# Optimization experiments

Measured on AMD Instinct MI355X. Metric: run time of the kernel, lower is better.

The kernel has to match this reference:

```python
import math
import jax, jax.numpy as jnp
import numpy as np

V, D, H, L, F, T, B = 32000, 1024, 16, 4, 4096, 1024, 2
HD = D // H
EPS = 1e-5


def make_pe(max_len, d):
    pos = np.arange(max_len)[:, None].astype(np.float32)
    div = np.exp(np.arange(0, d, 2).astype(np.float32) * (-math.log(10000.0) / d))
    pe = np.zeros((max_len, d), dtype=np.float32)
    pe[:, 0::2] = np.sin(pos * div)
    pe[:, 1::2] = np.cos(pos * div)
    return jnp.asarray(pe)


def setup_inputs() -> dict:
    key = jax.random.key(0)
    ks = jax.random.split(key, 12)
    s = 0.02
    inp = {
        'tokens': jax.random.randint(ks[0], (B, T), 0, V, dtype=jnp.int32),
        'mask': jnp.tril(jnp.ones((T, T), dtype=jnp.int32)),
        'emb': jax.random.normal(ks[1], (V, D), jnp.float32) * s,
        'pe': make_pe(T, D),
        'ln1_g': jnp.ones((L, D)), 'ln1_b': jnp.zeros((L, D)),
        'Wqkv': jax.random.normal(ks[2], (L, D, 3 * D), jnp.float32) * s,
        'bqkv': jnp.zeros((L, 3 * D)),
        'Wproj': jax.random.normal(ks[3], (L, D, D), jnp.float32) * s,
        'bproj': jnp.zeros((L, D)),
        'ln2_g': jnp.ones((L, D)), 'ln2_b': jnp.zeros((L, D)),
        'W1': jax.random.normal(ks[4], (L, D, F), jnp.float32) * s,
        'b1': jnp.zeros((L, F)),
        'W2': jax.random.normal(ks[5], (L, F, D), jnp.float32) * s,
        'b2': jnp.zeros((L, D)),
        'lnf_g': jnp.ones((D,)), 'lnf_b': jnp.zeros((D,)),
        'out_b': jnp.zeros((V,)),
    }
    return inp


def layer_norm(x, g, b):
    m = jnp.mean(x, axis=-1, keepdims=True)
    v = jnp.mean((x - m) ** 2, axis=-1, keepdims=True)
    return (x - m) / jnp.sqrt(v + EPS) * g + b


def attention(x, mask, Wqkv, bqkv, Wproj, bproj):
    b, t, c = x.shape
    qkv = (x @ Wqkv + bqkv).reshape(b, t, 3, H, HD)
    q, k, v = jnp.moveaxis(qkv, 2, 0)  # each [B,T,H,HD]
    q = q.transpose(0, 2, 1, 3)  # [B,H,T,HD]
    k = k.transpose(0, 2, 1, 3)
    v = v.transpose(0, 2, 1, 3)
    scores = jnp.einsum('bhqd,bhkd->bhqk', q, k) / math.sqrt(HD)
    scores = jnp.where(mask[None, None] == 0, -1e9, scores)
    attn = jax.nn.softmax(scores, axis=-1)
    out = jnp.einsum('bhqk,bhkd->bhqd', attn, v)
    out = out.transpose(0, 2, 1, 3).reshape(b, t, c)
    return out @ Wproj + bproj, attn


def reference(tokens, mask, emb, pe, ln1_g, ln1_b, Wqkv, bqkv, Wproj, bproj,
              ln2_g, ln2_b, W1, b1, W2, b2, lnf_g, lnf_b, out_b):
    x = emb[tokens] + pe[:tokens.shape[1]]
    attn = None
    for i in range(L):
        a, attn = attention(layer_norm(x, ln1_g[i], ln1_b[i]), mask,
                            Wqkv[i], bqkv[i], Wproj[i], bproj[i])
        x = x + a
        h = layer_norm(x, ln2_g[i], ln2_b[i])
        h = jax.nn.gelu(h @ W1[i] + b1[i], approximate=False) @ W2[i] + b2[i]
        x = x + h
    x = layer_norm(x, lnf_g, lnf_b)
    logits = x @ emb.T + out_b  # weight tying
    return logits, attn
```

## Files before the change

### kernel.cpp

```cpp
#include <hip/hip_runtime.h>
#include <cstdint>

#define DEV static __device__ __forceinline__

typedef unsigned short u16;
typedef __bf16 bf16x8 __attribute__((ext_vector_type(8)));
typedef float f32x4 __attribute__((ext_vector_type(4)));
typedef unsigned short u16x4 __attribute__((ext_vector_type(4)));

constexpr int V = 32000, D = 1024, H = 16, L = 4, F = 4096, T = 1024, B = 2;
constexpr int HD = 64;

DEV u16 f2bf(float f) {
    union { float f; uint32_t i; } c; c.f = f;
    uint32_t x = c.i;
    return (u16)((x + 0x7fffu + ((x >> 16) & 1u)) >> 16);
}
DEV bf16x8 ld8(const u16* p) { return *reinterpret_cast<const bf16x8*>(p); }

DEV void gl16(const void* g, void* l) {
    __builtin_amdgcn_global_load_lds((const __attribute__((address_space(1))) void*)g,
                                     (__attribute__((address_space(3))) void*)l, 16, 0, 0);
}

__global__ __launch_bounds__(256) void k_embln(const int* __restrict__ tok,
        const float* __restrict__ emb, const float* __restrict__ pe,
        const float* __restrict__ g, const float* __restrict__ b,
        float* __restrict__ x, u16* __restrict__ out) {
    int row = blockIdx.x, tid = threadIdx.x;
    int t = row & (T - 1);
    int vv = tok[row];
    f32x4 v = ((const f32x4*)(emb + (size_t)vv * D))[tid] + ((const f32x4*)(pe + (size_t)t * D))[tid];
    ((f32x4*)(x + (size_t)row * D))[tid] = v;
    float s = v[0] + v[1] + v[2] + v[3];
    float s2 = v[0]*v[0] + v[1]*v[1] + v[2]*v[2] + v[3]*v[3];
#pragma unroll
    for (int m = 1; m < 64; m <<= 1) { s += __shfl_xor(s, m); s2 += __shfl_xor(s2, m); }
    __shared__ float ps[4], ps2[4];
    int wave = tid >> 6;
    if ((tid & 63) == 0) { ps[wave] = s; ps2[wave] = s2; }
    __syncthreads();
    s = ps[0] + ps[1] + ps[2] + ps[3];
    s2 = ps2[0] + ps2[1] + ps2[2] + ps2[3];
    float mean = s * (1.f / D);
    float var = s2 * (1.f / D) - mean * mean;
    float r = rsqrtf(var + 1e-5f);
    f32x4 gg = ((const f32x4*)g)[tid];
    f32x4 bb = ((const f32x4*)b)[tid];
    u16x4 o;
#pragma unroll
    for (int j = 0; j < 4; j++) o[j] = f2bf((v[j] - mean) * r * gg[j] + bb[j]);
    ((u16x4*)(out + (size_t)row * D))[tid] = o;
}

template <int S>
__global__ __launch_bounds__(256) void k_redln(const float* __restrict__ pp,
        const float* __restrict__ bias, float* __restrict__ x,
        const float* __restrict__ g, const float* __restrict__ b,
        u16* __restrict__ out) {
    int row = blockIdx.x, tid = threadIdx.x;
    f32x4 v = ((const f32x4*)(x + (size_t)row * D))[tid];
#pragma unroll
    for (int s = 0; s < S; s++)
        v += ((const f32x4*)(pp + ((size_t)s * (B * T) + row) * D))[tid];
    v += ((const f32x4*)bias)[tid];
    ((f32x4*)(x + (size_t)row * D))[tid] = v;
    float s = v[0] + v[1] + v[2] + v[3];
    float s2 = v[0]*v[0] + v[1]*v[1] + v[2]*v[2] + v[3]*v[3];
#pragma unroll
    for (int m = 1; m < 64; m <<= 1) { s += __shfl_xor(s, m); s2 += __shfl_xor(s2, m); }
    __shared__ float ps[4], ps2[4];
    int wave = tid >> 6;
    if ((tid & 63) == 0) { ps[wave] = s; ps2[wave] = s2; }
    __syncthreads();
    s = ps[0] + ps[1] + ps[2] + ps[3];
    s2 = ps2[0] + ps2[1] + ps2[2] + ps2[3];
    float mean = s * (1.f / D);
    float var = s2 * (1.f / D) - mean * mean;
    float r = rsqrtf(var + 1e-5f);
    f32x4 gg = ((const f32x4*)g)[tid];
    f32x4 bb = ((const f32x4*)b)[tid];
    u16x4 o;
#pragma unroll
    for (int j = 0; j < 4; j++) o[j] = f2bf((v[j] - mean) * r * gg[j] + bb[j]);
    ((u16x4*)(out + (size_t)row * D))[tid] = o;
}

__global__ __launch_bounds__(256) void k_cast(const float* __restrict__ src,
        u16* __restrict__ dst) {
    int i = (blockIdx.x * 256 + threadIdx.x) * 4;
    f32x4 v = *(const f32x4*)(src + i);
    u16x4 o;
#pragma unroll
    for (int j = 0; j < 4; j++) o[j] = f2bf(v[j]);
    *(u16x4*)(dst + i) = o;
}

__global__ __launch_bounds__(256) void k_castT4(const float* __restrict__ Wqkv,
        const float* __restrict__ Wproj, const float* __restrict__ W1,
        const float* __restrict__ W2, u16* __restrict__ wt) {
    int bid = blockIdx.x;
    const float* src; u16* dst; int Rr, Cc, t;
    if (bid < 3072)      { src = Wqkv;  dst = wt;                   Rr = D; Cc = 3 * D; t = bid; }
    else if (bid < 4096) { src = Wproj; dst = wt + 3 * D * D;       Rr = D; Cc = D;     t = bid - 3072; }
    else if (bid < 8192) { src = W1;    dst = wt + 4 * D * D;       Rr = D; Cc = F;     t = bid - 4096; }
    else                 { src = W2;    dst = wt + 4 * D * D + D * F; Rr = F; Cc = D;   t = bid - 8192; }
    int ntx = Cc >> 5;
    int c0 = (t % ntx) * 32, r0 = (t / ntx) * 32;
    __shared__ u16 tl[32][33];
    int x = threadIdx.x & 31, y = threadIdx.x >> 5;
#pragma unroll
    for (int i = 0; i < 4; i++)
        tl[y + i * 8][x] = f2bf(src[(size_t)(r0 + y + i * 8) * Cc + c0 + x]);
    __syncthreads();
#pragma unroll
    for (int i = 0; i < 4; i++)
        dst[(size_t)(c0 + y + i * 8) * Rr + r0 + x] = tl[x][y + i * 8];
}

template <int EPI, bool VT>
__global__ __launch_bounds__(256) void k_gemm_bt(
        const u16* __restrict__ A, int lda,
        const u16* __restrict__ Bt, int ldb,
        const float* __restrict__ bias,
        void* __restrict__ Cv, int ldc, int K, u16* __restrict__ vT) {
    __shared__ u16 tA[2][128 * 32];
    __shared__ u16 tB[2][128 * 32];
    int gm = gridDim.x;
    int nwg = gm * gridDim.y;
    int orig = blockIdx.y * gm + blockIdx.x;
    int xcd = orig & 7, idx = orig >> 3;
    int q = nwg >> 3, rr = nwg & 7;
    int wg = (xcd < rr ? xcd * (q + 1) : rr * (q + 1) + (xcd - rr) * q) + idx;
    int m0 = (wg % gm) * 128, n0 = (wg / gm) * 128;
    int koff = (EPI == 4) ? blockIdx.z * K : 0;
    int tid = threadIdx.x, wave = tid >> 6, lane = tid & 63;
    int llo = lane & 15, lhi = lane >> 4;
    int wr = wave >> 1, wc = wave & 1;
    f32x4 acc[4][4] = {};
    int nk = K / 32;
    for (int c = wave; c < 8; c += 4) {
        int e = (c * 64 + lane) * 8;
        int row = e >> 5, col = e & 31;
        gl16(A  + (size_t)(m0 + row) * lda + koff + col, &tA[0][c * 512]);
        gl16(Bt + (size_t)(n0 + row) * ldb + koff + col, &tB[0][c * 512]);
    }
    __syncthreads();
    int cur = 0;
    for (int t = 0; t < nk; ++t) {
        if (t + 1 < nk) {
            int kk = koff + (t + 1) * 32;
            for (int c = wave; c < 8; c += 4) {
                int e = (c * 64 + lane) * 8;
                int row = e >> 5, col = e & 31;
                gl16(A  + (size_t)(m0 + row) * lda + kk + col, &tA[cur ^ 1][c * 512]);
                gl16(Bt + (size_t)(n0 + row) * ldb + kk + col, &tB[cur ^ 1][c * 512]);
            }
        }
        bf16x8 af[4], bfr[4];
#pragma unroll
        for (int mi = 0; mi < 4; mi++) af[mi] = ld8(&tA[cur][(wr * 64 + mi * 16 + llo) * 32 + lhi * 8]);
#pragma unroll
        for (int ni = 0; ni < 4; ni++) bfr[ni] = ld8(&tB[cur][(wc * 64 + ni * 16 + llo) * 32 + lhi * 8]);
#pragma unroll
        for (int mi = 0; mi < 4; mi++)
#pragma unroll
            for (int ni = 0; ni < 4; ni++)
                acc[mi][ni] = __builtin_amdgcn_mfma_f32_16x16x32_bf16(af[mi], bfr[ni], acc[mi][ni], 0, 0, 0);
        __syncthreads();
        cur ^= 1;
    }
#pragma unroll
    for (int ni = 0; ni < 4; ni++) {
        int col = n0 + wc * 64 + ni * 16 + llo;
        float bb = 0.f;
        if (EPI != 4) bb = bias[col];
#pragma unroll
        for (int mi = 0; mi < 4; mi++) {
            int row0 = m0 + wr * 64 + mi * 16 + lhi * 4;
            if (VT && col >= 2 * D) {
                int dv = col - 2 * D;
                int b_ = row0 >> 10, t_ = row0 & (T - 1);
                u16x4 pk;
#pragma unroll
                for (int r = 0; r < 4; r++) pk[r] = f2bf(acc[mi][ni][r] + bb);
                *(u16x4*)(vT + ((size_t)(b_ * 16 + (dv >> 6)) * HD + (dv & 63)) * T + t_) = pk;
            } else {
#pragma unroll
                for (int r = 0; r < 4; r++) {
                    int row = row0 + r;
                    float o = acc[mi][ni][r] + bb;
                    if (EPI == 1) o = 0.5f * o * (1.f + erff(o * 0.70710678118f));
                    if (EPI == 3) {
                        ((float*)Cv)[(size_t)row * ldc + col] = o;
                    } else if (EPI == 4) {
                        ((float*)Cv)[((size_t)blockIdx.z * (B * T) + row) * ldc + col] = o;
                    } else {
                        ((u16*)Cv)[(size_t)row * ldc + col] = f2bf(o);
                    }
                }
            }
        }
    }
}

DEV bf16x8 ldf(const u16* half, int row, int lhi) {
    int lb = row * 64 + lhi * 16;
    lb ^= ((lb >> 9) & 1) << 5;
    return *(const bf16x8*)((const char*)half + lb);
}
DEV void stg(const u16* gb, int ld, int kc, u16* dstBase, int wave, int lane) {
#pragma unroll
    for (int i = 0; i < 2; i++) {
        int p = (wave * 2 + i) * 64 + lane;
        int l = p ^ (((p >> 5) & 1) << 1);
        gl16(gb + (size_t)(l >> 2) * ld + kc + (l & 3) * 8, dstBase + (wave * 2 + i) * 512);
    }
}
#define SB_BAR() do { __builtin_amdgcn_sched_barrier(0); __builtin_amdgcn_s_barrier(); } while (0)

__global__ __launch_bounds__(512, 2) void k_gemm8(
        const u16* __restrict__ A, int lda,
        const u16* __restrict__ Bt, int ldb,
        const float* __restrict__ bias,
        float* __restrict__ C, int ldc, int K) {
    __shared__ u16 lds[2][4][256 * 32];
    int gm = gridDim.x, nwg = gm * gridDim.y;
    int orig = blockIdx.y * gm + blockIdx.x;
    int xcd = orig & 7, idx = orig >> 3;
    int q = nwg >> 3, rr = nwg & 7;
    int wg = (xcd < rr ? xcd * (q + 1) : rr * (q + 1) + (xcd - rr) * q) + idx;
    int m0 = (wg % gm) * 256, n0 = (wg / gm) * 256;
    int tid = threadIdx.x, wave = tid >> 6, lane = tid & 63;
    int llo = lane & 15, lhi = lane >> 4;
    int wm = wave >> 2, wn = wave & 3;
    const u16* Ab = A + (size_t)m0 * lda;
    const u16* Bb = Bt + (size_t)n0 * ldb;
    int nk = K >> 6;
    f32x4 acc[8][4] = {};
    stg(Ab, lda, 0,   &lds[0][0][0], wave, lane);
    stg(Bb, ldb, 0,   &lds[0][1][0], wave, lane);
    stg(Ab, lda, 32,  &lds[0][2][0], wave, lane);
    stg(Bb, ldb, 32,  &lds[0][3][0], wave, lane);
    stg(Ab, lda, 64,  &lds[1][0][0], wave, lane);
    stg(Bb, ldb, 64,  &lds[1][1][0], wave, lane);
    stg(Ab, lda, 96,  &lds[1][2][0], wave, lane);
    asm volatile("s_waitcnt vmcnt(10)");
    SB_BAR();
    for (int t = 0; t < nk; ++t) {
        const int bf = t & 1;
        bf16x8 af[8], b0, b1;
#pragma unroll
        for (int mi = 0; mi < 8; mi++) af[mi] = ldf(&lds[bf][0][0], wm * 128 + mi * 16 + llo, lhi);
        b0 = ldf(&lds[bf][1][0], wn * 64 + llo, lhi);
        b1 = ldf(&lds[bf][1][0], wn * 64 + 16 + llo, lhi);
        if (t + 1 < nk) stg(Bb, ldb, (t + 1) * 64 + 32, &lds[bf ^ 1][3][0], wave, lane);
        __builtin_amdgcn_s_setprio(1);
#pragma unroll
        for (int mi = 0; mi < 8; mi++) {
            acc[mi][0] = __builtin_amdgcn_mfma_f32_16x16x32_bf16(af[mi], b0, acc[mi][0], 0, 0, 0);
            acc[mi][1] = __builtin_amdgcn_mfma_f32_16x16x32_bf16(af[mi], b1, acc[mi][1], 0, 0, 0);
        }
        __builtin_amdgcn_s_setprio(0);
        SB_BAR();
        b0 = ldf(&lds[bf][1][0], wn * 64 + 32 + llo, lhi);
        b1 = ldf(&lds[bf][1][0], wn * 64 + 48 + llo, lhi);
        if (t + 2 < nk) stg(Ab, lda, (t + 2) * 64, &lds[bf][0][0], wave, lane);
        __builtin_amdgcn_s_setprio(1);
#pragma unroll
        for (int mi = 0; mi < 8; mi++) {
            acc[mi][2] = __builtin_amdgcn_mfma_f32_16x16x32_bf16(af[mi], b0, acc[mi][2], 0, 0, 0);
            acc[mi][3] = __builtin_amdgcn_mfma_f32_16x16x32_bf16(af[mi], b1, acc[mi][3], 0, 0, 0);
        }
        __builtin_amdgcn_s_setprio(0);
        if (t + 2 < nk)      { asm volatile("s_waitcnt vmcnt(10)"); }
        else if (t + 1 < nk) { asm volatile("s_waitcnt vmcnt(8)"); }
        else                 { asm volatile("s_waitcnt vmcnt(0)"); }
        SB_BAR();
#pragma unroll
        for (int mi = 0; mi < 8; mi++) af[mi] = ldf(&lds[bf][2][0], wm * 128 + mi * 16 + llo, lhi);
        b0 = ldf(&lds[bf][3][0], wn * 64 + llo, lhi);
        b1 = ldf(&lds[bf][3][0], wn * 64 + 16 + llo, lhi);
        if (t + 2 < nk) stg(Bb, ldb, (t + 2) * 64, &lds[bf][1][0], wave, lane);
        __builtin_amdgcn_s_setprio(1);
#pragma unroll
        for (int mi = 0; mi < 8; mi++) {
            acc[mi][0] = __builtin_amdgcn_mfma_f32_16x16x32_bf16(af[mi], b0, acc[mi][0], 0, 0, 0);
            acc[mi][1] = __builtin_amdgcn_mfma_f32_16x16x32_bf16(af[mi], b1, acc[mi][1], 0, 0, 0);
        }
        __builtin_amdgcn_s_setprio(0);
        SB_BAR();
        b0 = ldf(&lds[bf][3][0], wn * 64 + 32 + llo, lhi);
        b1 = ldf(&lds[bf][3][0], wn * 64 + 48 + llo, lhi);
        if (t + 2 < nk) stg(Ab, lda, (t + 2) * 64 + 32, &lds[bf][2][0], wave, lane);
        __builtin_amdgcn_s_setprio(1);
#pragma unroll
        for (int mi = 0; mi < 8; mi++) {
            acc[mi][2] = __builtin_amdgcn_mfma_f32_16x16x32_bf16(af[mi], b0, acc[mi][2], 0, 0, 0);
            acc[mi][3] = __builtin_amdgcn_mfma_f32_16x16x32_bf16(af[mi], b1, acc[mi][3], 0, 0, 0);
        }
        __builtin_amdgcn_s_setprio(0);
        if (t + 1 < nk) {
            if (t + 2 < nk) { asm volatile("s_waitcnt vmcnt(10)"); }
            else            { asm volatile("s_waitcnt vmcnt(4)"); }
        }
        SB_BAR();
    }
#pragma unroll
    for (int ni = 0; ni < 4; ni++) {
        int col = n0 + wn * 64 + ni * 16 + llo;
        float bb = bias[col];
#pragma unroll
        for (int mi = 0; mi < 8; mi++) {
            int row0 = m0 + wm * 128 + mi * 16 + lhi * 4;
#pragma unroll
            for (int r = 0; r < 4; r++)
                C[(size_t)(row0 + r) * ldc + col] = acc[mi][ni][r] + bb;
        }
    }
}

template <int PW>
__global__ __launch_bounds__(256) void k_fattn(const u16* __restrict__ qkv,
        const u16* __restrict__ vT, u16* __restrict__ out, float* __restrict__ attnF) {
    __shared__ u16 plds[4][16 * 40];
    int bh = blockIdx.y; int b = bh >> 4, h = bh & 15;
    int tid = threadIdx.x, wave = tid >> 6, lane = tid & 63;
    int llo = lane & 15, lhi = lane >> 4;
    int i0 = blockIdx.x * 64 + wave * 16;
    const u16* qb = qkv + (size_t)b * T * (3 * D) + h * HD;
    const u16* kb = qb + D;
    const u16* vt = vT + (size_t)bh * HD * T;
    bf16x8 q0 = ld8(qb + (size_t)(i0 + llo) * (3 * D) + lhi * 8);
    bf16x8 q1 = ld8(qb + (size_t)(i0 + llo) * (3 * D) + 32 + lhi * 8);
    int qrow = i0 + llo;
    float m = -3e38f, s = 0.f;
    f32x4 oacc[4] = {};
    u16* pw = &plds[wave][0];
    for (int k0 = 0; k0 < i0 + 16; k0 += 32) {
        f32x4 sc0 = {}, sc1 = {};
        {
            bf16x8 kf0 = ld8(kb + (size_t)(k0 + llo) * (3 * D) + lhi * 8);
            bf16x8 kf1 = ld8(kb + (size_t)(k0 + llo) * (3 * D) + 32 + lhi * 8);
            sc0 = __builtin_amdgcn_mfma_f32_16x16x32_bf16(kf0, q0, sc0, 0, 0, 0);
            sc0 = __builtin_amdgcn_mfma_f32_16x16x32_bf16(kf1, q1, sc0, 0, 0, 0);
        }
        if (k0 + 16 < i0 + 16) {
            bf16x8 kf0 = ld8(kb + (size_t)(k0 + 16 + llo) * (3 * D) + lhi * 8);
            bf16x8 kf1 = ld8(kb + (size_t)(k0 + 16 + llo) * (3 * D) + 32 + lhi * 8);
            sc1 = __builtin_amdgcn_mfma_f32_16x16x32_bf16(kf0, q0, sc1, 0, 0, 0);
            sc1 = __builtin_amdgcn_mfma_f32_16x16x32_bf16(kf1, q1, sc1, 0, 0, 0);
        }
        float vv[8]; float mx = m;
#pragma unroll
        for (int hf = 0; hf < 2; hf++)
#pragma unroll
            for (int r = 0; r < 4; r++) {
                int k = k0 + hf * 16 + lhi * 4 + r;
                float x = (hf ? sc1[r] : sc0[r]) * 0.125f;
                float v = (k <= qrow) ? x : -3e38f;
                vv[hf * 4 + r] = v;
                mx = fmaxf(mx, v);
            }
        mx = fmaxf(mx, __shfl_xor(mx, 16));
        mx = fmaxf(mx, __shfl_xor(mx, 32));
        float p[8]; float ps = 0.f;
#pragma unroll
        for (int j = 0; j < 8; j++) { p[j] = __expf(vv[j] - mx); ps += p[j]; }
        ps += __shfl_xor(ps, 16);
        ps += __shfl_xor(ps, 32);
        float scale = __expf(m - mx);
        s = s * scale + ps;
        m = mx;
        float sr[4];
#pragma unroll
        for (int r = 0; r < 4; r++) sr[r] = __shfl(scale, lhi * 4 + r);
#pragma unroll
        for (int n = 0; n < 4; n++)
#pragma unroll
            for (int r = 0; r < 4; r++) oacc[n][r] *= sr[r];
#pragma unroll
        for (int hf = 0; hf < 2; hf++) {
            u16x4 pk;
#pragma unroll
            for (int r = 0; r < 4; r++) pk[r] = f2bf(p[hf * 4 + r]);
            *(u16x4*)(pw + llo * 40 + hf * 16 + lhi * 4) = pk;
        }
        bf16x8 pa = ld8(pw + llo * 40 + lhi * 8);
#pragma unroll
        for (int n = 0; n < 4; n++) {
            bf16x8 vb = ld8(vt + (size_t)(n * 16 + llo) * T + k0 + lhi * 8);
            oacc[n] = __builtin_amdgcn_mfma_f32_16x16x32_bf16(pa, vb, oacc[n], 0, 0, 0);
        }
    }
    float inv = 1.f / s;
    float ir[4];
#pragma unroll
    for (int r = 0; r < 4; r++) ir[r] = __shfl(inv, lhi * 4 + r);
#pragma unroll
    for (int n = 0; n < 4; n++)
#pragma unroll
        for (int r = 0; r < 4; r++) {
            int i = i0 + lhi * 4 + r, c = n * 16 + llo;
            out[(size_t)(b * T + i) * D + h * HD + c] = f2bf(oacc[n][r] * ir[r]);
        }
    if (PW) {
        float* ar = attnF + ((size_t)bh * T + qrow) * T;
        for (int j0 = 0; j0 < T; j0 += 16) {
            f32x4 pv = {};
            if (j0 <= qrow) {
                if (j0 < i0 + 16) {
                    bf16x8 kf0 = ld8(kb + (size_t)(j0 + llo) * (3 * D) + lhi * 8);
                    bf16x8 kf1 = ld8(kb + (size_t)(j0 + llo) * (3 * D) + 32 + lhi * 8);
                    f32x4 sc = {};
                    sc = __builtin_amdgcn_mfma_f32_16x16x32_bf16(kf0, q0, sc, 0, 0, 0);
                    sc = __builtin_amdgcn_mfma_f32_16x16x32_bf16(kf1, q1, sc, 0, 0, 0);
#pragma unroll
                    for (int r = 0; r < 4; r++) {
                        int j = j0 + lhi * 4 + r;
                        pv[r] = (j <= qrow) ? __expf(sc[r] * 0.125f - m) * inv : 0.f;
                    }
                }
            }
            *(f32x4*)(ar + j0 + lhi * 4) = pv;
        }
    }
}

extern "C" void kernel_launch(void* const* d_in, const int* in_sizes, int n_in,
                              void* d_out, int out_size, void* d_ws, size_t ws_size,
                              hipStream_t stream) {
    const int*   tok   = (const int*)d_in[0];
    const float* emb   = (const float*)d_in[2];
    const float* pe    = (const float*)d_in[3];
    const float* ln1g  = (const float*)d_in[4];
    const float* ln1b  = (const float*)d_in[5];
    const float* Wqkv  = (const float*)d_in[6];
    const float* bqkv  = (const float*)d_in[7];
    const float* Wproj = (const float*)d_in[8];
    const float* bproj = (const float*)d_in[9];
    const float* ln2g  = (const float*)d_in[10];
    const float* ln2b  = (const float*)d_in[11];
    const float* W1    = (const float*)d_in[12];
    const float* b1    = (const float*)d_in[13];
    const float* W2    = (const float*)d_in[14];
    const float* b2    = (const float*)d_in[15];
    const float* lnfg  = (const float*)d_in[16];
    const float* lnfb  = (const float*)d_in[17];
    const float* outb  = (const float*)d_in[18];

    float* logits  = (float*)d_out;
    float* attnF   = logits + (size_t)B * T * V;

    char* w = (char*)d_ws;
    float* x    = (float*)w;  w += (size_t)B * T * D * 4;
    u16* lnout  = (u16*)w;    w += (size_t)B * T * D * 2;
    u16* qkv    = (u16*)w;    w += (size_t)B * T * 3 * D * 2;
    u16* vT     = (u16*)w;    w += (size_t)B * H * HD * T * 2;
    u16* aout   = (u16*)w;    w += (size_t)B * T * D * 2;
    char* tail = w;
    u16* hmid   = (u16*)w;    w += (size_t)B * T * F * 2;
    u16* WTL    = (u16*)w;    w += (size_t)(5 * D * D + 2 * D * F) * 2;
    float* pp   = (float*)w;  w += (size_t)4 * B * T * D * 4;
    u16* embB   = (u16*)tail;

    dim3 blk(256);
    k_embln<<<dim3(B * T), blk, 0, stream>>>(tok, emb, pe, ln1g, ln1b, x, lnout);

    for (int l = 0; l < L; l++) {
        k_castT4<<<dim3(12288), blk, 0, stream>>>(
            Wqkv + (size_t)l * D * 3 * D, Wproj + (size_t)l * D * D,
            W1 + (size_t)l * D * F, W2 + (size_t)l * F * D, WTL);
        k_gemm_bt<0, true><<<dim3(B * T / 128, 3 * D / 128), blk, 0, stream>>>(
            lnout, D, WTL, D, bqkv + l * 3 * D, qkv, 3 * D, D, vT);
        if (l == L - 1)
            k_fattn<1><<<dim3(T / 64, B * H), blk, 0, stream>>>(qkv, vT, aout, attnF);
        else
            k_fattn<0><<<dim3(T / 64, B * H), blk, 0, stream>>>(qkv, vT, aout, attnF);
        k_gemm_bt<4, false><<<dim3(B * T / 128, D / 128, 2), blk, 0, stream>>>(
            aout, D, WTL + (size_t)3 * D * D, D, nullptr, pp, D, D / 2, nullptr);
        k_redln<2><<<dim3(B * T), blk, 0, stream>>>(pp, bproj + l * D, x,
            ln2g + l * D, ln2b + l * D, lnout);
        k_gemm_bt<1, false><<<dim3(B * T / 128, F / 128), blk, 0, stream>>>(
            lnout, D, WTL + (size_t)4 * D * D, D, b1 + l * F, hmid, F, D, nullptr);
        k_gemm_bt<4, false><<<dim3(B * T / 128, D / 128, 4), blk, 0, stream>>>(
            hmid, F, WTL + (size_t)4 * D * D + D * F, F, nullptr, pp, D, F / 4, nullptr);
        const float* ng = (l == L - 1) ? lnfg : ln1g + (l + 1) * D;
        const float* nb = (l == L - 1) ? lnfb : ln1b + (l + 1) * D;
        k_redln<4><<<dim3(B * T), blk, 0, stream>>>(pp, b2 + l * D, x, ng, nb, lnout);
    }
    k_cast<<<dim3(V * D / 1024), blk, 0, stream>>>(emb, embB);
    k_gemm8<<<dim3(B * T / 256, V / 256), dim3(512), 0, stream>>>(
        lnout, D, embB, D, outb, logits, V, D);
}
```

Baseline: 1.069 ms.

## Rewrite 128x128 layer GEMM with swizzled LDS and fine-grained ping-pong pipeline

Replaces the simple double-buffered 128x128 layer GEMM with a version modelled on the existing 256x256 logits kernel. It uses 64-wide K steps split into four 32-wide half-tiles, XOR-swizzled LDS addressing, staggered global-to-LDS loads issued between MFMA groups, explicit vmcnt waits, s_setprio and sched barriers. It also adds an occupancy hint of two blocks per CU. The goal is to hide load latency and cut LDS bank conflicts in the QKV, projection and MLP GEMMs, at the cost of fragile hand-counted wait counts.

```diff
diff --git a/kernel.cpp b/kernel.cpp
--- a/kernel.cpp
+++ b/kernel.cpp
@@ -118,16 +118,29 @@
         dst[(size_t)(c0 + y + i * 8) * Rr + r0 + x] = tl[x][y + i * 8];
 }
 
+DEV bf16x8 ldf(const u16* half, int row, int lhi) {
+    int lb = row * 64 + lhi * 16;
+    lb ^= ((lb >> 9) & 1) << 5;
+    return *(const bf16x8*)((const char*)half + lb);
+}
+DEV void stg(const u16* gb, int ld, int kc, u16* dstBase, int wave, int lane) {
+#pragma unroll
+    for (int i = 0; i < 2; i++) {
+        int p = (wave * 2 + i) * 64 + lane;
+        int l = p ^ (((p >> 5) & 1) << 1);
+        gl16(gb + (size_t)(l >> 2) * ld + kc + (l & 3) * 8, dstBase + (wave * 2 + i) * 512);
+    }
+}
+#define SB_BAR() do { __builtin_amdgcn_sched_barrier(0); __builtin_amdgcn_s_barrier(); } while (0)
+
 template <int EPI, bool VT>
-__global__ __launch_bounds__(256) void k_gemm_bt(
+__global__ __launch_bounds__(256, 2) void k_gemm4(
         const u16* __restrict__ A, int lda,
         const u16* __restrict__ Bt, int ldb,
         const float* __restrict__ bias,
         void* __restrict__ Cv, int ldc, int K, u16* __restrict__ vT) {
-    __shared__ u16 tA[2][128 * 32];
-    __shared__ u16 tB[2][128 * 32];
-    int gm = gridDim.x;
-    int nwg = gm * gridDim.y;
+    __shared__ u16 lds[2][4][128 * 32];
+    int gm = gridDim.x, nwg = gm * gridDim.y;
     int orig = blockIdx.y * gm + blockIdx.x;
     int xcd = orig & 7, idx = orig >> 3;
     int q = nwg >> 3, rr = nwg & 7;
@@ -136,48 +149,87 @@
     int koff = (EPI == 4) ? blockIdx.z * K : 0;
     int tid = threadIdx.x, wave = tid >> 6, lane = tid & 63;
     int llo = lane & 15, lhi = lane >> 4;
-    int wr = wave >> 1, wc = wave & 1;
+    int wm = wave >> 1, wn = wave & 1;
+    const u16* Ab = A + (size_t)m0 * lda;
+    const u16* Bb = Bt + (size_t)n0 * ldb;
+    int nk = K >> 6;
     f32x4 acc[4][4] = {};
-    int nk = K / 32;
-    for (int c = wave; c < 8; c += 4) {
-        int e = (c * 64 + lane) * 8;
-        int row = e >> 5, col = e & 31;
-        gl16(A  + (size_t)(m0 + row) * lda + koff + col, &tA[0][c * 512]);
-        gl16(Bt + (size_t)(n0 + row) * ldb + koff + col, &tB[0][c * 512]);
-    }
-    __syncthreads();
-    int cur = 0;
+    stg(Ab, lda, koff + 0,   &lds[0][0][0], wave, lane);
+    stg(Bb, ldb, koff + 0,   &lds[0][1][0], wave, lane);
+    stg(Ab, lda, koff + 32,  &lds[0][2][0], wave, lane);
+    stg(Bb, ldb, koff + 32,  &lds[0][3][0], wave, lane);
+    stg(Ab, lda, koff + 64,  &lds[1][0][0], wave, lane);
+    stg(Bb, ldb, koff + 64,  &lds[1][1][0], wave, lane);
+    stg(Ab, lda, koff + 96,  &lds[1][2][0], wave, lane);
+    asm volatile("s_waitcnt vmcnt(10)");
+    SB_BAR();
     for (int t = 0; t < nk; ++t) {
+        const int bf = t & 1;
+        bf16x8 af[4], b0, b1;
+#pragma unroll
+        for (int mi = 0; mi < 4; mi++) af[mi] = ldf(&lds[bf][0][0], wm * 64 + mi * 16 + llo, lhi);
+        b0 = ldf(&lds[bf][1][0], wn * 64 + llo, lhi);
+        b1 = ldf(&lds[bf][1][0], wn * 64 + 16 + llo, lhi);
+        if (t + 1 < nk) stg(Bb, ldb, koff + (t + 1) * 64 + 32, &lds[bf ^ 1][3][0], wave, lane);
+        __builtin_amdgcn_s_setprio(1);
+#pragma unroll
+        for (int mi = 0; mi < 4; mi++) {
+            acc[mi][0] = __builtin_amdgcn_mfma_f32_16x16x32_bf16(af[mi], b0, acc[mi][0], 0, 0, 0);
+            acc[mi][1] = __builtin_amdgcn_mfma_f32_16x16x32_bf16(af[mi], b1, acc[mi][1], 0, 0, 0);
+        }
+        __builtin_amdgcn_s_setprio(0);
+        SB_BAR();
+        b0 = ldf(&lds[bf][1][0], wn * 64 + 32 + llo, lhi);
+        b1 = ldf(&lds[bf][1][0], wn * 64 + 48 + llo, lhi);
+        if (t + 2 < nk) stg(Ab, lda, koff + (t + 2) * 64, &lds[bf][0][0], wave, lane);
+        __builtin_amdgcn_s_setprio(1);
+#pragma unroll
+        for (int mi = 0; mi < 4; mi++) {
+            acc[mi][2] = __builtin_amdgcn_mfma_f32_16x16x32_bf16(af[mi], b0, acc[mi][2], 0, 0, 0);
+            acc[mi][3] = __builtin_amdgcn_mfma_f32_16x16x32_bf16(af[mi], b1, acc[mi][3], 0, 0, 0);
+        }
+        __builtin_amdgcn_s_setprio(0);
+        if (t + 2 < nk)      { asm volatile("s_waitcnt vmcnt(10)"); }
+        else if (t + 1 < nk) { asm volatile("s_waitcnt vmcnt(8)"); }
+        else                 { asm volatile("s_waitcnt vmcnt(0)"); }
+        SB_BAR();
+#pragma unroll
+        for (int mi = 0; mi < 4; mi++) af[mi] = ldf(&lds[bf][2][0], wm * 64 + mi * 16 + llo, lhi);
+        b0 = ldf(&lds[bf][3][0], wn * 64 + llo, lhi);
+        b1 = ldf(&lds[bf][3][0], wn * 64 + 16 + llo, lhi);
+        if (t + 2 < nk) stg(Bb, ldb, koff + (t + 2) * 64, &lds[bf][1][0], wave, lane);
+        __builtin_amdgcn_s_setprio(1);
+#pragma unroll
+        for (int mi = 0; mi < 4; mi++) {
+            acc[mi][0] = __builtin_amdgcn_mfma_f32_16x16x32_bf16(af[mi], b0, acc[mi][0], 0, 0, 0);
+            acc[mi][1] = __builtin_amdgcn_mfma_f32_16x16x32_bf16(af[mi], b1, acc[mi][1], 0, 0, 0);
+        }
+        __builtin_amdgcn_s_setprio(0);
+        SB_BAR();
+        b0 = ldf(&lds[bf][3][0], wn * 64 + 32 + llo, lhi);
+        b1 = ldf(&lds[bf][3][0], wn * 64 + 48 + llo, lhi);
+        if (t + 2 < nk) stg(Ab, lda, koff + (t + 2) * 64 + 32, &lds[bf][2][0], wave, lane);
+        __builtin_amdgcn_s_setprio(1);
+#pragma unroll
+        for (int mi = 0; mi < 4; mi++) {
+            acc[mi][2] = __builtin_amdgcn_mfma_f32_16x16x32_bf16(af[mi], b0, acc[mi][2], 0, 0, 0);
+            acc[mi][3] = __builtin_amdgcn_mfma_f32_16x16x32_bf16(af[mi], b1, acc[mi][3], 0, 0, 0);
+        }
+        __builtin_amdgcn_s_setprio(0);
         if (t + 1 < nk) {
-            int kk = koff + (t + 1) * 32;
-            for (int c = wave; c < 8; c += 4) {
-                int e = (c * 64 + lane) * 8;
-                int row = e >> 5, col = e & 31;
-                gl16(A  + (size_t)(m0 + row) * lda + kk + col, &tA[cur ^ 1][c * 512]);
-                gl16(Bt + (size_t)(n0 + row) * ldb + kk + col, &tB[cur ^ 1][c * 512]);
-            }
-        }
-        bf16x8 af[4], bfr[4];
-#pragma unroll
-        for (int mi = 0; mi < 4; mi++) af[mi] = ld8(&tA[cur][(wr * 64 + mi * 16 + llo) * 32 + lhi * 8]);
-#pragma unroll
-        for (int ni = 0; ni < 4; ni++) bfr[ni] = ld8(&tB[cur][(wc * 64 + ni * 16 + llo) * 32 + lhi * 8]);
-#pragma unroll
-        for (int mi = 0; mi < 4; mi++)
-#pragma unroll
-            for (int ni = 0; ni < 4; ni++)
-                acc[mi][ni] = __builtin_amdgcn_mfma_f32_16x16x32_bf16(af[mi], bfr[ni], acc[mi][ni], 0, 0, 0);
-        __syncthreads();
-        cur ^= 1;
+            if (t + 2 < nk) { asm volatile("s_waitcnt vmcnt(10)"); }
+            else            { asm volatile("s_waitcnt vmcnt(4)"); }
+        }
+        SB_BAR();
     }
 #pragma unroll
     for (int ni = 0; ni < 4; ni++) {
-        int col = n0 + wc * 64 + ni * 16 + llo;
+        int col = n0 + wn * 64 + ni * 16 + llo;
         float bb = 0.f;
         if (EPI != 4) bb = bias[col];
 #pragma unroll
         for (int mi = 0; mi < 4; mi++) {
-            int row0 = m0 + wr * 64 + mi * 16 + lhi * 4;
+            int row0 = m0 + wm * 64 + mi * 16 + lhi * 4;
             if (VT && col >= 2 * D) {
                 int dv = col - 2 * D;
                 int b_ = row0 >> 10, t_ = row0 & (T - 1);
@@ -191,9 +243,7 @@
                     int row = row0 + r;
                     float o = acc[mi][ni][r] + bb;
                     if (EPI == 1) o = 0.5f * o * (1.f + erff(o * 0.70710678118f));
-                    if (EPI == 3) {
-                        ((float*)Cv)[(size_t)row * ldc + col] = o;
-                    } else if (EPI == 4) {
+                    if (EPI == 4) {
                         ((float*)Cv)[((size_t)blockIdx.z * (B * T) + row) * ldc + col] = o;
                     } else {
                         ((u16*)Cv)[(size_t)row * ldc + col] = f2bf(o);
@@ -203,21 +253,6 @@
         }
     }
 }
-
-DEV bf16x8 ldf(const u16* half, int row, int lhi) {
-    int lb = row * 64 + lhi * 16;
-    lb ^= ((lb >> 9) & 1) << 5;
-    return *(const bf16x8*)((const char*)half + lb);
-}
-DEV void stg(const u16* gb, int ld, int kc, u16* dstBase, int wave, int lane) {
-#pragma unroll
-    for (int i = 0; i < 2; i++) {
-        int p = (wave * 2 + i) * 64 + lane;
-        int l = p ^ (((p >> 5) & 1) << 1);
-        gl16(gb + (size_t)(l >> 2) * ld + kc + (l & 3) * 8, dstBase + (wave * 2 + i) * 512);
-    }
-}
-#define SB_BAR() do { __builtin_amdgcn_sched_barrier(0); __builtin_amdgcn_s_barrier(); } while (0)
 
 __global__ __launch_bounds__(512, 2) void k_gemm8(
         const u16* __restrict__ A, int lda,
@@ -471,19 +506,19 @@
         k_castT4<<<dim3(12288), blk, 0, stream>>>(
             Wqkv + (size_t)l * D * 3 * D, Wproj + (size_t)l * D * D,
             W1 + (size_t)l * D * F, W2 + (size_t)l * F * D, WTL);
-        k_gemm_bt<0, true><<<dim3(B * T / 128, 3 * D / 128), blk, 0, stream>>>(
+        k_gemm4<0, true><<<dim3(B * T / 128, 3 * D / 128), blk, 0, stream>>>(
             lnout, D, WTL, D, bqkv + l * 3 * D, qkv, 3 * D, D, vT);
         if (l == L - 1)
             k_fattn<1><<<dim3(T / 64, B * H), blk, 0, stream>>>(qkv, vT, aout, attnF);
         else
             k_fattn<0><<<dim3(T / 64, B * H), blk, 0, stream>>>(qkv, vT, aout, attnF);
-        k_gemm_bt<4, false><<<dim3(B * T / 128, D / 128, 2), blk, 0, stream>>>(
+        k_gemm4<4, false><<<dim3(B * T / 128, D / 128, 2), blk, 0, stream>>>(
             aout, D, WTL + (size_t)3 * D * D, D, nullptr, pp, D, D / 2, nullptr);
         k_redln<2><<<dim3(B * T), blk, 0, stream>>>(pp, bproj + l * D, x,
             ln2g + l * D, ln2b + l * D, lnout);
-        k_gemm_bt<1, false><<<dim3(B * T / 128, F / 128), blk, 0, stream>>>(
+        k_gemm4<1, false><<<dim3(B * T / 128, F / 128), blk, 0, stream>>>(
             lnout, D, WTL + (size_t)4 * D * D, D, b1 + l * F, hmid, F, D, nullptr);
-        k_gemm_bt<4, false><<<dim3(B * T / 128, D / 128, 4), blk, 0, stream>>>(
+        k_gemm4<4, false><<<dim3(B * T / 128, D / 128, 4), blk, 0, stream>>>(
             hmid, F, WTL + (size_t)4 * D * D + D * F, F, nullptr, pp, D, F / 4, nullptr);
         const float* ng = (l == L - 1) ? lnfg : ln1g + (l + 1) * D;
         const float* nb = (l == L - 1) ? lnfb : ln1b + (l + 1) * D;
```

Measured after the change: 996.2 us. 1.07x faster.
